# Optimization experiments

Hardware: AMD Instinct MI355X
Metric: run time of the kernel (lower is better)

Reference implementation:

```python
import jax, jax.numpy as jnp
import numpy as np

H = 8          # para_heads
LN_EPS = 1e-5  # torch LayerNorm default


def setup_inputs() -> dict:
    key = jax.random.key(0)
    ks = jax.random.split(key, 8)
    N, L, E, F = 32, 4096, 512, 2048
    D = E // H
    s = lambda fan_in: 1.0 / np.sqrt(fan_in)
    return {
        "Cp": jax.random.normal(ks[0], (N, L, E), jnp.float32),
        "W1": jax.random.normal(ks[1], (E, E), jnp.float32) * s(E),
        "W2": jax.random.normal(ks[2], (1, D), jnp.float32) * s(D),
        "W3": jax.random.normal(ks[3], (E, E), jnp.float32) * s(E),
        "Wf1": jax.random.normal(ks[4], (F, E), jnp.float32) * s(E),
        "bf1": jnp.zeros((F,), jnp.float32),
        "Wf2": jax.random.normal(ks[5], (E, F), jnp.float32) * s(F),
        "bf2": jnp.zeros((E,), jnp.float32),
        "gamma": jnp.ones((E,), jnp.float32),
        "beta": jnp.zeros((E,), jnp.float32),
    }


def reference(Cp, W1, W2, W3, Wf1, bf1, Wf2, bf2, gamma, beta):
    N, L, E = Cp.shape
    D = E // H
    # W1 projection: [N, L, E]
    CpW1 = jnp.einsum('nle,fe->nlf', Cp, W1)
    # raw row-major reshape as in the original (NOT a head transpose)
    head_split = CpW1.reshape(N, H, L, D)
    # W2 scores -> [N, H, L, 1]; softmax over size-1 dim yields ones (faithful)
    scores = jax.nn.softmax(jnp.einsum('nhld,od->nhlo', head_split, W2), axis=-1)
    # weighted sum over seq: [N, H, D]
    phi = jnp.einsum('nhld,nhlo->nhd', head_split, scores).reshape(N, E)
    w3_out = phi @ W3.T                                    # [N, E]
    fwd = jax.nn.relu(w3_out @ Wf1.T + bf1) @ Wf2.T + bf2  # FFN
    x = w3_out + fwd
    mu = jnp.mean(x, axis=-1, keepdims=True)
    var = jnp.mean(jnp.square(x - mu), axis=-1, keepdims=True)
    out = (x - mu) * jax.lax.rsqrt(var + LN_EPS) * gamma + beta
    return out  # dropout is identity in eval mode
```

## Files before the change

kernel.cpp:

```cpp
#include <hip/hip_runtime.h>
#include <hip/hip_bf16.h>

#define NN 32
#define LL 4096
#define EE 512
#define HH 8
#define DD 64
#define FF 2048
#define CC 8

__global__ void k_prep(const float* __restrict__ Cp, const float* __restrict__ W1,
                       float* __restrict__ P, float* __restrict__ V) {
    int bid = blockIdx.x;
    int tid = threadIdx.x;
    if (bid < 2048) {
        int c = bid & 7;
        int h = (bid >> 3) & 7;
        int n = bid >> 6;
        const float4* base = reinterpret_cast<const float4*>(
            Cp + ((size_t)n * LL + (size_t)h * 512 + (size_t)c * 64) * EE) + tid;
        float ax = 0.f, ay = 0.f, az = 0.f, aw = 0.f;
#pragma unroll 8
        for (int r = 0; r < 64; ++r) {
            float4 v = base[(size_t)r * (EE / 4)];
            ax += v.x; ay += v.y; az += v.z; aw += v.w;
        }
        float4 o; o.x = ax; o.y = ay; o.z = az; o.w = aw;
        reinterpret_cast<float4*>(P + (((size_t)c * NN + n) * HH + h) * EE)[tid] = o;
    } else {
        int gid2 = (bid - 2048) * 128 + tid;
#pragma unroll
        for (int rep = 0; rep < 2; ++rep) {
            int idx = gid2 + rep * 4096;
            int d = idx >> 7;
            int e4 = idx & 127;
            float ax = 0.f, ay = 0.f, az = 0.f, aw = 0.f;
#pragma unroll
            for (int j = 0; j < 8; ++j) {
                float4 v = reinterpret_cast<const float4*>(
                    W1 + (size_t)(j * 64 + d) * EE)[e4];
                ax += v.x; ay += v.y; az += v.z; aw += v.w;
            }
            float4 o; o.x = ax; o.y = ay; o.z = az; o.w = aw;
            reinterpret_cast<float4*>(V + (size_t)d * EE)[e4] = o;
        }
    }
}

__global__ void k_phi(const float* __restrict__ P, const float* __restrict__ V,
                      float* __restrict__ phi) {
    __shared__ float S[EE];
    __shared__ float red[256];
    int n = blockIdx.x >> 3;
    int h = blockIdx.x & 7;
    for (int e = threadIdx.x; e < EE; e += 256) {
        float s = 0.f;
#pragma unroll
        for (int c = 0; c < CC; ++c)
            s += P[(((size_t)c * NN + n) * HH + h) * EE + e];
        S[e] = s;
    }
    __syncthreads();
    int d  = threadIdx.x >> 2;
    int ch = threadIdx.x & 3;
    const float* Vr = V + (size_t)d * EE + ch * 128;
    const float* Sr = S + ch * 128;
    float acc = 0.f;
#pragma unroll 4
    for (int e = 0; e < 128; ++e) acc += Sr[e] * Vr[e];
    red[threadIdx.x] = acc;
    __syncthreads();
    if (threadIdx.x < DD) {
        int dd = threadIdx.x;
        float r = red[dd * 4] + red[dd * 4 + 1] + red[dd * 4 + 2] + red[dd * 4 + 3];
        phi[(size_t)n * EE + h * DD + dd] = r;
    }
}

template<int K, int F, int NG, int FPW, int MODE>
__global__ __launch_bounds__(256) void k_gemm(const float* __restrict__ A,
                                              const float* __restrict__ W,
                                              const float* __restrict__ bias,
                                              const float* __restrict__ res,
                                              float* __restrict__ out) {
    constexpr int V4 = K / 256;
    int wid  = (blockIdx.x * 256 + threadIdx.x) >> 6;
    int lane = threadIdx.x & 63;
    constexpr int NGROUPS = NN / NG;
    int ng = wid % NGROUPS;
    int fc = wid / NGROUPS;
    int n0 = ng * NG;
    int f0 = fc * FPW;

    float4 a4[NG][V4];
#pragma unroll
    for (int g = 0; g < NG; ++g)
#pragma unroll
        for (int k = 0; k < V4; ++k)
            a4[g][k] = reinterpret_cast<const float4*>(
                A + (size_t)(n0 + g) * K)[k * 64 + lane];

#pragma unroll
    for (int fi = 0; fi < FPW; ++fi) {
        int f = f0 + fi;
        float4 w4[V4];
#pragma unroll
        for (int k = 0; k < V4; ++k)
            w4[k] = reinterpret_cast<const float4*>(
                W + (size_t)f * K)[k * 64 + lane];
        float acc[NG];
#pragma unroll
        for (int g = 0; g < NG; ++g) {
            float s = 0.f;
#pragma unroll
            for (int k = 0; k < V4; ++k) {
                s += a4[g][k].x * w4[k].x + a4[g][k].y * w4[k].y
                   + a4[g][k].z * w4[k].z + a4[g][k].w * w4[k].w;
            }
#pragma unroll
            for (int m = 32; m > 0; m >>= 1) s += __shfl_xor(s, m);
            acc[g] = s;
        }
        if (lane == 0) {
            float b = (MODE == 0) ? 0.f : bias[f];
#pragma unroll
            for (int g = 0; g < NG; ++g) {
                float v = acc[g] + b;
                if (MODE == 1) v = fmaxf(v, 0.f);
                if (MODE == 2) v += res[(size_t)(n0 + g) * F + f];
                out[(size_t)(n0 + g) * F + f] = v;
            }
        }
    }
}

__global__ void k_ln(const float* __restrict__ x, const float* __restrict__ gamma,
                     const float* __restrict__ beta, float* __restrict__ out) {
    __shared__ float wred[4];
    int n = blockIdx.x;
    int tid = threadIdx.x;
    float a = x[(size_t)n * EE + tid];
    float b = x[(size_t)n * EE + 256 + tid];
    float s = a + b;
#pragma unroll
    for (int off = 32; off > 0; off >>= 1) s += __shfl_down(s, off);
    int wid = tid >> 6;
    if ((tid & 63) == 0) wred[wid] = s;
    __syncthreads();
    if (tid == 0) wred[0] = (wred[0] + wred[1] + wred[2] + wred[3]) * (1.0f / EE);
    __syncthreads();
    float mu = wred[0];
    float da = a - mu, db = b - mu;
    float q = da * da + db * db;
#pragma unroll
    for (int off = 32; off > 0; off >>= 1) q += __shfl_down(q, off);
    __syncthreads();
    if ((tid & 63) == 0) wred[wid] = q;
    __syncthreads();
    if (tid == 0) wred[0] = (wred[0] + wred[1] + wred[2] + wred[3]) * (1.0f / EE);
    __syncthreads();
    float var = wred[0];
    float rstd = rsqrtf(var + 1e-5f);
    out[(size_t)n * EE + tid]       = da * rstd * gamma[tid] + beta[tid];
    out[(size_t)n * EE + 256 + tid] = db * rstd * gamma[tid + 256] + beta[tid + 256];
}

extern "C" void kernel_launch(void* const* d_in, const int* in_sizes, int n_in,
                              void* d_out, int out_size, void* d_ws, size_t ws_size,
                              hipStream_t stream) {
    const float* Cp    = (const float*)d_in[0];
    const float* W1    = (const float*)d_in[1];
    const float* W3    = (const float*)d_in[3];
    const float* Wf1   = (const float*)d_in[4];
    const float* bf1   = (const float*)d_in[5];
    const float* Wf2   = (const float*)d_in[6];
    const float* bf2   = (const float*)d_in[7];
    const float* gamma = (const float*)d_in[8];
    const float* beta  = (const float*)d_in[9];
    float* out = (float*)d_out;

    float* ws  = (float*)d_ws;
    float* P   = ws;
    float* V   = P + (size_t)CC * NN * HH * EE;
    float* phi = V + (size_t)DD * EE;
    float* w3  = phi + (size_t)NN * EE;
    float* h1  = w3 + (size_t)NN * EE;
    float* x   = h1 + (size_t)NN * FF;

    k_prep<<<2048 + 32, 128, 0, stream>>>(Cp, W1, P, V);
    k_phi<<<NN * HH, 256, 0, stream>>>(P, V, phi);
    k_gemm<EE, EE, 8, 2, 0><<<256, 256, 0, stream>>>(phi, W3, nullptr, nullptr, w3);
    k_gemm<EE, FF, 8, 2, 1><<<1024, 256, 0, stream>>>(w3, Wf1, bf1, nullptr, h1);
    k_gemm<FF, EE, 4, 1, 2><<<1024, 256, 0, stream>>>(h1, Wf2, bf2, w3, x);
    k_ln<<<NN, 256, 0, stream>>>(x, gamma, beta, out);
}
```

Baseline: 77.41 us.

## Fuse phi and W3 projection, restructure Cp reduction with nontemporal loads

```diff
diff --git a/kernel.cpp b/kernel.cpp
--- a/kernel.cpp
+++ b/kernel.cpp
@@ -7,74 +7,108 @@
 #define HH 8
 #define DD 64
 #define FF 2048
-#define CC 8
-
-__global__ void k_prep(const float* __restrict__ Cp, const float* __restrict__ W1,
-                       float* __restrict__ P, float* __restrict__ V) {
-    int bid = blockIdx.x;
-    int tid = threadIdx.x;
-    if (bid < 2048) {
-        int c = bid & 7;
-        int h = (bid >> 3) & 7;
-        int n = bid >> 6;
-        const float4* base = reinterpret_cast<const float4*>(
-            Cp + ((size_t)n * LL + (size_t)h * 512 + (size_t)c * 64) * EE) + tid;
+
+typedef float f32x4 __attribute__((ext_vector_type(4)));
+
+__global__ __launch_bounds__(256) void k_prep(const float* __restrict__ Cp,
+                                              const float* __restrict__ W1,
+                                              float* __restrict__ P,
+                                              float* __restrict__ V) {
+    __shared__ f32x4 sh[128];
+    int b = blockIdx.x;
+    int t = threadIdx.x;
+    if (b < 1024) {
+        int n   = b >> 5;
+        int sub = b & 31;
+        int h   = sub >> 2;
+        int q   = sub & 3;
+        int e4  = t & 127;
+        int half = t >> 7;
+        const f32x4* base = reinterpret_cast<const f32x4*>(Cp) +
+            (size_t)(n * LL + sub * 128 + half) * (EE / 4) + e4;
         float ax = 0.f, ay = 0.f, az = 0.f, aw = 0.f;
 #pragma unroll 8
         for (int r = 0; r < 64; ++r) {
-            float4 v = base[(size_t)r * (EE / 4)];
+            f32x4 v = __builtin_nontemporal_load(base + (size_t)r * 2 * (EE / 4));
             ax += v.x; ay += v.y; az += v.z; aw += v.w;
         }
-        float4 o; o.x = ax; o.y = ay; o.z = az; o.w = aw;
-        reinterpret_cast<float4*>(P + (((size_t)c * NN + n) * HH + h) * EE)[tid] = o;
+        if (half) { f32x4 o; o.x = ax; o.y = ay; o.z = az; o.w = aw; sh[e4] = o; }
+        __syncthreads();
+        if (!half) {
+            f32x4 o = sh[e4];
+            o.x += ax; o.y += ay; o.z += az; o.w += aw;
+            reinterpret_cast<f32x4*>(P)[(size_t)((q * NN + n) * HH + h) * 128 + e4] = o;
+        }
     } else {
-        int gid2 = (bid - 2048) * 128 + tid;
-#pragma unroll
-        for (int rep = 0; rep < 2; ++rep) {
-            int idx = gid2 + rep * 4096;
-            int d = idx >> 7;
-            int e4 = idx & 127;
-            float ax = 0.f, ay = 0.f, az = 0.f, aw = 0.f;
-#pragma unroll
-            for (int j = 0; j < 8; ++j) {
-                float4 v = reinterpret_cast<const float4*>(
-                    W1 + (size_t)(j * 64 + d) * EE)[e4];
-                ax += v.x; ay += v.y; az += v.z; aw += v.w;
-            }
-            float4 o; o.x = ax; o.y = ay; o.z = az; o.w = aw;
-            reinterpret_cast<float4*>(V + (size_t)d * EE)[e4] = o;
-        }
-    }
-}
-
-__global__ void k_phi(const float* __restrict__ P, const float* __restrict__ V,
-                      float* __restrict__ phi) {
-    __shared__ float S[EE];
+        int idx = (b - 1024) * 256 + t;
+        int d = idx >> 7, e4 = idx & 127;
+        float vx = 0.f, vy = 0.f, vz = 0.f, vw = 0.f;
+#pragma unroll
+        for (int j = 0; j < 8; ++j) {
+            f32x4 v = reinterpret_cast<const f32x4*>(
+                W1 + (size_t)(j * 64 + d) * EE)[e4];
+            vx += v.x; vy += v.y; vz += v.z; vw += v.w;
+        }
+        f32x4 o; o.x = vx; o.y = vy; o.z = vz; o.w = vw;
+        reinterpret_cast<f32x4*>(V)[(size_t)d * 128 + e4] = o;
+    }
+}
+
+__global__ __launch_bounds__(256) void k_phiw3(const float* __restrict__ P,
+                                               const float* __restrict__ V,
+                                               const float* __restrict__ W3,
+                                               float* __restrict__ w3) {
+    __shared__ float S[HH * EE];
+    __shared__ float ph[EE];
     __shared__ float red[256];
-    int n = blockIdx.x >> 3;
-    int h = blockIdx.x & 7;
-    for (int e = threadIdx.x; e < EE; e += 256) {
-        float s = 0.f;
-#pragma unroll
-        for (int c = 0; c < CC; ++c)
-            s += P[(((size_t)c * NN + n) * HH + h) * EE + e];
-        S[e] = s;
-    }
-    __syncthreads();
-    int d  = threadIdx.x >> 2;
-    int ch = threadIdx.x & 3;
-    const float* Vr = V + (size_t)d * EE + ch * 128;
-    const float* Sr = S + ch * 128;
+    int n = blockIdx.x >> 2;
+    int j = blockIdx.x & 3;
+    int t = threadIdx.x;
+
+    f32x4* S4 = reinterpret_cast<f32x4*>(S);
+    const f32x4* P4 = reinterpret_cast<const f32x4*>(P);
+#pragma unroll
+    for (int c = 0; c < 4; ++c) {
+        int idx = c * 256 + t;
+        f32x4 a = P4[(size_t)(0 * NN + n) * 1024 + idx];
+        f32x4 b = P4[(size_t)(1 * NN + n) * 1024 + idx];
+        f32x4 d = P4[(size_t)(2 * NN + n) * 1024 + idx];
+        f32x4 e = P4[(size_t)(3 * NN + n) * 1024 + idx];
+        a.x += b.x + d.x + e.x; a.y += b.y + d.y + e.y;
+        a.z += b.z + d.z + e.z; a.w += b.w + d.w + e.w;
+        S4[idx] = a;
+    }
+    __syncthreads();
+
+#pragma unroll
+    for (int rep = 0; rep < 2; ++rep) {
+        int o = t + rep * 256;
+        int h = o >> 6, d = o & 63;
+        const f32x4* Vr = reinterpret_cast<const f32x4*>(V) + (size_t)d * 128;
+        const f32x4* Sr = reinterpret_cast<const f32x4*>(S) + (size_t)h * 128;
+        float acc = 0.f;
+#pragma unroll 4
+        for (int k = 0; k < 128; ++k) {
+            f32x4 s = Sr[k], v = Vr[k];
+            acc += s.x * v.x + s.y * v.y + s.z * v.z + s.w * v.w;
+        }
+        ph[o] = acc;
+    }
+    __syncthreads();
+
+    int f  = j * 128 + (t >> 1);
+    int eh = t & 1;
+    const f32x4* Wr = reinterpret_cast<const f32x4*>(W3) + (size_t)f * 128 + eh * 64;
+    const f32x4* Pr = reinterpret_cast<const f32x4*>(ph) + eh * 64;
     float acc = 0.f;
 #pragma unroll 4
-    for (int e = 0; e < 128; ++e) acc += Sr[e] * Vr[e];
-    red[threadIdx.x] = acc;
-    __syncthreads();
-    if (threadIdx.x < DD) {
-        int dd = threadIdx.x;
-        float r = red[dd * 4] + red[dd * 4 + 1] + red[dd * 4 + 2] + red[dd * 4 + 3];
-        phi[(size_t)n * EE + h * DD + dd] = r;
-    }
+    for (int k = 0; k < 64; ++k) {
+        f32x4 p = Pr[k], w = Wr[k];
+        acc += p.x * w.x + p.y * w.y + p.z * w.z + p.w * w.w;
+    }
+    red[t] = acc;
+    __syncthreads();
+    if (t < 128) w3[(size_t)n * EE + j * 128 + t] = red[2 * t] + red[2 * t + 1];
 }
 
 template<int K, int F, int NG, int FPW, int MODE>
@@ -178,18 +212,16 @@
     const float* gamma = (const float*)d_in[8];
     const float* beta  = (const float*)d_in[9];
     float* out = (float*)d_out;
-
     float* ws  = (float*)d_ws;
-    float* P   = ws;
-    float* V   = P + (size_t)CC * NN * HH * EE;
-    float* phi = V + (size_t)DD * EE;
-    float* w3  = phi + (size_t)NN * EE;
-    float* h1  = w3 + (size_t)NN * EE;
-    float* x   = h1 + (size_t)NN * FF;
-
-    k_prep<<<2048 + 32, 128, 0, stream>>>(Cp, W1, P, V);
-    k_phi<<<NN * HH, 256, 0, stream>>>(P, V, phi);
-    k_gemm<EE, EE, 8, 2, 0><<<256, 256, 0, stream>>>(phi, W3, nullptr, nullptr, w3);
+
+    float* P  = ws;
+    float* V  = P + (size_t)4 * NN * HH * EE;
+    float* w3 = V + (size_t)DD * EE;
+    float* h1 = w3 + (size_t)NN * EE;
+    float* x  = h1 + (size_t)NN * FF;
+
+    k_prep<<<1024 + 32, 256, 0, stream>>>(Cp, W1, P, V);
+    k_phiw3<<<NN * 4, 256, 0, stream>>>(P, V, W3, w3);
     k_gemm<EE, FF, 8, 2, 1><<<1024, 256, 0, stream>>>(w3, Wf1, bf1, nullptr, h1);
     k_gemm<FF, EE, 4, 1, 2><<<1024, 256, 0, stream>>>(h1, Wf2, bf2, w3, x);
     k_ln<<<NN, 256, 0, stream>>>(x, gamma, beta, out);
```

New measurement: 102.3 us. 1.32x slower.
